# Performance work log

Measured on AMD Instinct MI355X. Metric: run time of the kernel, lower is better.

## Reference

```python
import jax, jax.numpy as jnp
import numpy as np

B, S, D = 4, 4096, 1024

def setup_inputs() -> dict:
    key = jax.random.key(0)
    ks = jax.random.split(key, 7)
    s = 1.0 / np.sqrt(D)
    return {
        "x":   jax.random.normal(ks[0], (B, S, D), dtype=jnp.float32),
        "Wq":  jax.random.uniform(ks[1], (D, D), jnp.float32, -s, s),
        "bq":  jax.random.uniform(ks[2], (D,),   jnp.float32, -s, s),
        "Wk":  jax.random.uniform(ks[3], (D, D), jnp.float32, -s, s),
        "bk":  jax.random.uniform(ks[4], (D,),   jnp.float32, -s, s),
        "Wv":  jax.random.uniform(ks[5], (D, D), jnp.float32, -s, s),
        "bv":  jax.random.uniform(ks[6], (D,),   jnp.float32, -s, s),
    }

def reference(x, Wq, bq, Wk, bk, Wv, bv):
    # Linear projections (torch Linear: x @ W.T + b; here W stored as [in, out])
    Q = jnp.einsum('bsd,df->bsf', x, Wq) + bq
    K = jnp.einsum('bsd,df->bsf', x, Wk) + bk
    V = jnp.einsum('bsd,df->bsf', x, Wv) + bv
    scale = 1.0 / jnp.sqrt(jnp.asarray(D, dtype=jnp.float32))
    scores = jnp.einsum('bqd,bkd->bqk', Q, K) * scale  # [B, S, S]
    attn = jax.nn.softmax(scores, axis=-1)
    return jnp.einsum('bqk,bkd->bqd', attn, V)
```

## Files before the change

### kernel.cpp

```cpp
#include <hip/hip_runtime.h>
#include <hip/hip_bf16.h>
#include <stdint.h>


typedef __attribute__((ext_vector_type(8))) short bf16x8;
typedef __attribute__((ext_vector_type(4))) float f32x4;

static __device__ __forceinline__ unsigned short f2b(float f) {
  union { float f; unsigned u; } x; x.f = f;
  unsigned u = x.u;
  u += 0x7fffu + ((u >> 16) & 1u);
  return (unsigned short)(u >> 16);
}
static __device__ __forceinline__ float b2f(unsigned short s) {
  union { unsigned u; float f; } x; x.u = ((unsigned)s) << 16;
  return x.f;
}

static __device__ __forceinline__ void gl_lds16(const void* g, void* l) {
  __builtin_amdgcn_global_load_lds(
      (const __attribute__((address_space(1))) void*)(uintptr_t)(g),
      (__attribute__((address_space(3))) void*)(uint32_t)(uintptr_t)(l),
      16, 0, 0);
}

__global__ void convert_x(const float* __restrict__ in,
                          unsigned short* __restrict__ out, int n8) {
  int i = blockIdx.x * blockDim.x + threadIdx.x;
  if (i >= n8) return;
  const float4* p = (const float4*)in + (size_t)i * 2;
  float4 a = p[0], b = p[1];
  bf16x8 o;
  o[0] = (short)f2b(a.x); o[1] = (short)f2b(a.y);
  o[2] = (short)f2b(a.z); o[3] = (short)f2b(a.w);
  o[4] = (short)f2b(b.x); o[5] = (short)f2b(b.y);
  o[6] = (short)f2b(b.z); o[7] = (short)f2b(b.w);
  ((bf16x8*)out)[i] = o;
}

__global__ void transpose_w(const float* __restrict__ in,
                            unsigned short* __restrict__ out) {
  __shared__ float tile[32][33];
  const int tx = threadIdx.x;
  const int x = blockIdx.x * 32 + tx;
  const int y0 = blockIdx.y * 32;
  for (int j = threadIdx.y; j < 32; j += 8)
    tile[j][tx] = in[(size_t)(y0 + j) * 1024 + x];
  __syncthreads();
  const int ox = blockIdx.y * 32 + tx;
  const int oy0 = blockIdx.x * 32;
  for (int j = threadIdx.y; j < 32; j += 8)
    out[(size_t)(oy0 + j) * 1024 + ox] = f2b(tile[tx][j]);
}

template <int OUTF>
__global__ __launch_bounds__(512, 2)
void gemm256(const unsigned short* __restrict__ A, long lda, long sAz,
             const unsigned short* __restrict__ B, long ldb, long sBz,
             void* __restrict__ Cv, long ldc, long sCz,
             const float* __restrict__ bias, int bias_mode,
             int K, float alpha) {
  __shared__ __align__(16) unsigned short As[2][2][8192];
  __shared__ __align__(16) unsigned short Bs[2][2][8192];

  const unsigned gx = gridDim.x, gy = gridDim.y;
  const unsigned nwg = gx * gy * gridDim.z;
  const unsigned hwid = (blockIdx.z * gy + blockIdx.y) * gx + blockIdx.x;
  unsigned tile = hwid;
  if ((nwg & 7u) == 0u) tile = (hwid & 7u) * (nwg >> 3) + (hwid >> 3);
  const unsigned bxi = tile % gx;
  const unsigned byi = (tile / gx) % gy;
  const unsigned bzi = tile / (gx * gy);

  const int t = threadIdx.x;
  const int wid = t >> 6, lane = t & 63;
  const int wm = wid >> 2, wn = wid & 3;
  const int fr = lane & 15, fq = lane >> 4;
  const long bm = (long)byi * 256;
  const long bn = (long)bxi * 256;
  const unsigned short* Ab = A + (size_t)bzi * sAz;
  const unsigned short* Bb = B + (size_t)bzi * sBz;

  const int srow = t >> 2;
  const int soct8 = (((t & 3) ^ ((t >> 3) & 3))) * 8;
  const unsigned short* AgS = Ab + (bm + srow) * lda + soct8;
  const unsigned short* BgS = Bb + (bn + srow) * ldb + soct8;
  const int dstw = wid * 512;
  const int rs16 = (fq ^ ((fr >> 1) & 3)) << 4;

  const int NT = K >> 6;
  f32x4 acc[8][4] = {};

  auto stg = [&](const unsigned short* GS, long ld, unsigned short* region,
                 int kt, int kh) {
    const unsigned short* s0 = GS + (size_t)kt * 64 + kh * 32;
    gl_lds16(s0, region + dstw);
    gl_lds16(s0 + (size_t)128 * ld, region + 4096 + dstw);
  };
  auto rdA = [&](int buf, int kh, int i) {
    return *(const bf16x8*)((const char*)&As[buf][kh][0] +
                            (wm * 128 + i * 16 + fr) * 64 + rs16);
  };
  auto rdB = [&](int buf, int kh, int j) {
    return *(const bf16x8*)((const char*)&Bs[buf][kh][0] +
                            (wn * 64 + j * 16 + fr) * 64 + rs16);
  };

  stg(AgS, lda, &As[0][0][0], 0, 0); stg(BgS, ldb, &Bs[0][0][0], 0, 0);
  stg(AgS, lda, &As[0][1][0], 0, 1); stg(BgS, ldb, &Bs[0][1][0], 0, 1);
  asm volatile("s_waitcnt vmcnt(4)" ::: "memory");
  asm volatile("s_barrier" ::: "memory");

#define PHASE(kh)                                                             \
  do {                                                                        \
    if (tt + 1 < NT) {                                                        \
      stg(AgS, lda, &As[nb][kh][0], tt + 1, kh);                              \
      stg(BgS, ldb, &Bs[nb][kh][0], tt + 1, kh);                              \
    }                                                                         \
    bf16x8 bfr[4], ar[2], arn[2];                                             \
    _Pragma("unroll")                                                         \
    for (int j = 0; j < 4; ++j) bfr[j] = rdB(cb, kh, j);                      \
    ar[0] = rdA(cb, kh, 0); ar[1] = rdA(cb, kh, 1);                           \
    __builtin_amdgcn_s_setprio(1);                                            \
    _Pragma("unroll")                                                         \
    for (int p = 0; p < 4; ++p) {                                             \
      if (p < 3) {                                                            \
        arn[0] = rdA(cb, kh, p * 2 + 2);                                      \
        arn[1] = rdA(cb, kh, p * 2 + 3);                                      \
      }                                                                       \
      _Pragma("unroll")                                                       \
      for (int ii = 0; ii < 2; ++ii)                                          \
        _Pragma("unroll")                                                     \
        for (int j = 0; j < 4; ++j)                                           \
          acc[p * 2 + ii][j] = __builtin_amdgcn_mfma_f32_16x16x32_bf16(       \
              ar[ii], bfr[j], acc[p * 2 + ii][j], 0, 0, 0);                   \
      if (p < 3) { ar[0] = arn[0]; ar[1] = arn[1]; }                          \
    }                                                                         \
    __builtin_amdgcn_s_setprio(0);                                            \
  } while (0)

  for (int tt = 0; tt < NT; ++tt) {
    const int cb = tt & 1, nb = (tt + 1) & 1;
    if (tt > 0) {
      asm volatile("s_waitcnt vmcnt(4)" ::: "memory");
      asm volatile("s_barrier" ::: "memory");
    }
    PHASE(0);
    if (tt + 1 < NT) {
      asm volatile("s_waitcnt vmcnt(4)" ::: "memory");
    } else {
      asm volatile("s_waitcnt vmcnt(0)" ::: "memory");
    }
    asm volatile("s_barrier" ::: "memory");
    PHASE(1);
  }
#undef PHASE

  char* Cb = (char*)Cv + (size_t)bzi * sCz * (OUTF ? 4 : 2);
  const long crow0 = bm + wm * 128 + fq * 4;
  const long ccol0 = bn + wn * 64 + fr;
#pragma unroll
  for (int i = 0; i < 8; ++i) {
#pragma unroll
    for (int j = 0; j < 4; ++j) {
      const long col = ccol0 + j * 16;
      float badd_c = (bias_mode == 1) ? bias[col] : 0.0f;
#pragma unroll
      for (int r = 0; r < 4; ++r) {
        const long row = crow0 + i * 16 + r;
        float v = acc[i][j][r] * alpha + badd_c;
        if (bias_mode == 2) v += bias[row];
        if (OUTF)
          ((float*)Cb)[row * ldc + col] = v;
        else
          ((unsigned short*)Cb)[row * ldc + col] = f2b(v);
      }
    }
  }
}

__global__ __launch_bounds__(256)
void softmax_rows(unsigned short* __restrict__ S) {
  const int t = threadIdx.x;
  unsigned short* row = S + (size_t)blockIdx.x * 4096;
  const bf16x8* p = (const bf16x8*)row;
  bf16x8 u0 = p[t * 2], u1 = p[t * 2 + 1];

  float v[16];
  float m = -1e30f;
#pragma unroll
  for (int j = 0; j < 8; j++) { v[j] = b2f((unsigned short)u0[j]); }
#pragma unroll
  for (int j = 0; j < 8; j++) { v[8 + j] = b2f((unsigned short)u1[j]); }
#pragma unroll
  for (int j = 0; j < 16; j++) m = fmaxf(m, v[j]);

#pragma unroll
  for (int off = 32; off > 0; off >>= 1) m = fmaxf(m, __shfl_xor(m, off));
  __shared__ float redm[4];
  if ((t & 63) == 0) redm[t >> 6] = m;
  __syncthreads();
  m = fmaxf(fmaxf(redm[0], redm[1]), fmaxf(redm[2], redm[3]));

  float s = 0.0f;
#pragma unroll
  for (int j = 0; j < 16; j++) { v[j] = __expf(v[j] - m); s += v[j]; }
#pragma unroll
  for (int off = 32; off > 0; off >>= 1) s += __shfl_xor(s, off);
  __shared__ float reds[4];
  if ((t & 63) == 0) reds[t >> 6] = s;
  __syncthreads();
  s = reds[0] + reds[1] + reds[2] + reds[3];
  const float inv = 1.0f / s;

  bf16x8 o0, o1;
#pragma unroll
  for (int j = 0; j < 8; j++) o0[j] = (short)f2b(v[j] * inv);
#pragma unroll
  for (int j = 0; j < 8; j++) o1[j] = (short)f2b(v[8 + j] * inv);
  bf16x8* q = (bf16x8*)row;
  q[t * 2] = o0;
  q[t * 2 + 1] = o1;
}

extern "C" void kernel_launch(void* const* d_in, const int* in_sizes, int n_in,
                              void* d_out, int out_size, void* d_ws,
                              size_t ws_size, hipStream_t stream) {
  const float* x  = (const float*)d_in[0];
  const float* Wq = (const float*)d_in[1];
  const float* bq = (const float*)d_in[2];
  const float* Wk = (const float*)d_in[3];
  const float* bk = (const float*)d_in[4];
  const float* Wv = (const float*)d_in[5];
  const float* bv = (const float*)d_in[6];
  float* out = (float*)d_out;

  const int Bb = 4, S = 4096, D = 1024;
  const long BS = (long)Bb * S;
  const size_t MiB = 1u << 20;

  char* base = (char*)d_ws;
  unsigned short* Wqt = (unsigned short*)(base);
  unsigned short* Wkt = (unsigned short*)(base + 2 * MiB);
  unsigned short* Wvt = (unsigned short*)(base + 4 * MiB);
  unsigned short* Qb  = (unsigned short*)(base + 6 * MiB);
  unsigned short* Kb  = (unsigned short*)(base + 38 * MiB);
  unsigned short* Vt  = (unsigned short*)(base + 70 * MiB);
  unsigned short* xb  = (unsigned short*)(base + 102 * MiB);
  unsigned short* Sb  = xb;
  const bool batched = ws_size >= (size_t)(102 + 128) * MiB;

  const int n8 = (int)(BS * D / 8);
  convert_x<<<n8 / 256, 256, 0, stream>>>(x, xb, n8);

  dim3 tb(32, 8), tg(32, 32);
  transpose_w<<<tg, tb, 0, stream>>>(Wq, Wqt);
  transpose_w<<<tg, tb, 0, stream>>>(Wk, Wkt);
  transpose_w<<<tg, tb, 0, stream>>>(Wv, Wvt);

  gemm256<0><<<dim3(D / 256, BS / 256, 1), 512, 0, stream>>>(
      xb, D, 0, Wqt, D, 0, Qb, D, 0, bq, 1, D, 1.0f);
  gemm256<0><<<dim3(D / 256, BS / 256, 1), 512, 0, stream>>>(
      xb, D, 0, Wkt, D, 0, Kb, D, 0, bk, 1, D, 1.0f);
  gemm256<0><<<dim3(BS / 256, D / 256, 1), 512, 0, stream>>>(
      Wvt, D, 0, xb, D, 0, Vt, BS, 0, bv, 2, D, 1.0f);

  const float scale = 0.03125f;
  if (batched) {
    gemm256<0><<<dim3(S / 256, S / 256, Bb), 512, 0, stream>>>(
        Qb, D, (long)S * D, Kb, D, (long)S * D, Sb, S, (long)S * S,
        nullptr, 0, D, scale);
    softmax_rows<<<Bb * S, 256, 0, stream>>>(Sb);
    gemm256<1><<<dim3(D / 256, S / 256, Bb), 512, 0, stream>>>(
        Sb, S, (long)S * S, Vt, BS, (long)S, out, D, (long)S * D,
        nullptr, 0, S, 1.0f);
  } else {
    for (int b = 0; b < Bb; b++) {
      const unsigned short* Qp = Qb + (long)b * S * D;
      const unsigned short* Kp = Kb + (long)b * S * D;
      gemm256<0><<<dim3(S / 256, S / 256, 1), 512, 0, stream>>>(
          Qp, D, 0, Kp, D, 0, Sb, S, 0, nullptr, 0, D, scale);
      softmax_rows<<<S, 256, 0, stream>>>(Sb);
      gemm256<1><<<dim3(D / 256, S / 256, 1), 512, 0, stream>>>(
          Sb, S, 0, Vt + (long)b * S, BS, 0, out + (long)b * S * D, D, 0,
          nullptr, 0, S, 1.0f);
    }
  }
}
```

Measured before the change: 483.5 us.

## Restructure GEMM main loop into 8-phase ping-pong schedule with staggered A/B loads

Replaces the two-half-K double-buffered loop with a schedule that processes two K-tiles per iteration in four sub-phases each. Each sub-phase issues a slice of the next global-to-LDS copies, then hits a barrier, then runs its MFMAs. The LDS layout changes from split 32-wide K halves to full 64-wide rows with an XOR swizzle on 16-byte chunks. The goal is to interleave the memory traffic more finely with the MFMA work and keep B prefetched further ahead. In exchange there are more barriers per tile, and the hand-written vmcnt accounting is fragile. The loop also assumes NT is even.

Measured after the change: 460.4 us. 4.8% less time.

```diff
diff --git a/kernel.cpp b/kernel.cpp
--- a/kernel.cpp
+++ b/kernel.cpp
@@ -53,6 +53,8 @@
     out[(size_t)(oy0 + j) * 1024 + ox] = f2b(tile[tx][j]);
 }
 
+#define MFMA16(a, b, c) __builtin_amdgcn_mfma_f32_16x16x32_bf16(a, b, c, 0, 0, 0)
+
 template <int OUTF>
 __global__ __launch_bounds__(512, 2)
 void gemm256(const unsigned short* __restrict__ A, long lda, long sAz,
@@ -60,17 +62,17 @@
              void* __restrict__ Cv, long ldc, long sCz,
              const float* __restrict__ bias, int bias_mode,
              int K, float alpha) {
-  __shared__ __align__(16) unsigned short As[2][2][8192];
-  __shared__ __align__(16) unsigned short Bs[2][2][8192];
+  __shared__ __align__(16) unsigned short As[2][256 * 64];
+  __shared__ __align__(16) unsigned short Bs[2][256 * 64];
 
   const unsigned gx = gridDim.x, gy = gridDim.y;
   const unsigned nwg = gx * gy * gridDim.z;
   const unsigned hwid = (blockIdx.z * gy + blockIdx.y) * gx + blockIdx.x;
-  unsigned tile = hwid;
-  if ((nwg & 7u) == 0u) tile = (hwid & 7u) * (nwg >> 3) + (hwid >> 3);
-  const unsigned bxi = tile % gx;
-  const unsigned byi = (tile / gx) % gy;
-  const unsigned bzi = tile / (gx * gy);
+  unsigned tileid = hwid;
+  if ((nwg & 7u) == 0u) tileid = (hwid & 7u) * (nwg >> 3) + (hwid >> 3);
+  const unsigned bxi = tileid % gx;
+  const unsigned byi = (tileid / gx) % gy;
+  const unsigned bzi = tileid / (gx * gy);
 
   const int t = threadIdx.x;
   const int wid = t >> 6, lane = t & 63;
@@ -81,78 +83,96 @@
   const unsigned short* Ab = A + (size_t)bzi * sAz;
   const unsigned short* Bb = B + (size_t)bzi * sBz;
 
-  const int srow = t >> 2;
-  const int soct8 = (((t & 3) ^ ((t >> 3) & 3))) * 8;
-  const unsigned short* AgS = Ab + (bm + srow) * lda + soct8;
-  const unsigned short* BgS = Bb + (bn + srow) * ldb + soct8;
-  const int dstw = wid * 512;
-  const int rs16 = (fq ^ ((fr >> 1) & 3)) << 4;
+  const int sr = t >> 3;
+  const int scol = 8 * ((t & 7) ^ (sr & 7));
+  const unsigned short* AgS = Ab + (bm + sr) * lda + scol;
+  const unsigned short* BgS = Bb + (bn + sr) * ldb + scol;
+  const int ldsw = wid * 512;
 
   const int NT = K >> 6;
   f32x4 acc[8][4] = {};
 
-  auto stg = [&](const unsigned short* GS, long ld, unsigned short* region,
-                 int kt, int kh) {
-    const unsigned short* s0 = GS + (size_t)kt * 64 + kh * 32;
-    gl_lds16(s0, region + dstw);
-    gl_lds16(s0 + (size_t)128 * ld, region + 4096 + dstw);
+  auto SH = [&](const unsigned short* GS, long ld, int kt, int h,
+                unsigned short* dstbuf) {
+    const unsigned short* s = GS + (size_t)(h * 128) * ld + (size_t)kt * 64;
+    gl_lds16(s, dstbuf + h * 128 * 64 + ldsw);
+    gl_lds16(s + (size_t)64 * ld, dstbuf + (h * 128 + 64) * 64 + ldsw);
   };
-  auto rdA = [&](int buf, int kh, int i) {
-    return *(const bf16x8*)((const char*)&As[buf][kh][0] +
-                            (wm * 128 + i * 16 + fr) * 64 + rs16);
+
+  auto rdA = [&](int buf, int m, int kh) {
+    const int row = wm * 128 + m * 16 + fr;
+    const int inb = (kh * 64 + fq * 16) ^ ((fr & 7) << 4);
+    return *(const bf16x8*)((const char*)&As[buf][0] + row * 128 + inb);
   };
-  auto rdB = [&](int buf, int kh, int j) {
-    return *(const bf16x8*)((const char*)&Bs[buf][kh][0] +
-                            (wn * 64 + j * 16 + fr) * 64 + rs16);
+  auto rdB = [&](int buf, int j, int kh) {
+    const int row = wn * 64 + j * 16 + fr;
+    const int inb = (kh * 64 + fq * 16) ^ ((fr & 7) << 4);
+    return *(const bf16x8*)((const char*)&Bs[buf][0] + row * 128 + inb);
   };
 
-  stg(AgS, lda, &As[0][0][0], 0, 0); stg(BgS, ldb, &Bs[0][0][0], 0, 0);
-  stg(AgS, lda, &As[0][1][0], 0, 1); stg(BgS, ldb, &Bs[0][1][0], 0, 1);
-  asm volatile("s_waitcnt vmcnt(4)" ::: "memory");
-  asm volatile("s_barrier" ::: "memory");
-
-#define PHASE(kh)                                                             \
-  do {                                                                        \
-    if (tt + 1 < NT) {                                                        \
-      stg(AgS, lda, &As[nb][kh][0], tt + 1, kh);                              \
-      stg(BgS, ldb, &Bs[nb][kh][0], tt + 1, kh);                              \
+#define PHASE(CB, P, STAGES, WAITS)                                           \
+  {                                                                           \
+    if ((P) == 0) {                                                           \
+      _Pragma("unroll") for (int j = 0; j < 4; ++j) {                         \
+        bfr[j][0] = rdB(CB, j, 0);                                            \
+        bfr[j][1] = rdB(CB, j, 1);                                            \
+      }                                                                       \
     }                                                                         \
-    bf16x8 bfr[4], ar[2], arn[2];                                             \
-    _Pragma("unroll")                                                         \
-    for (int j = 0; j < 4; ++j) bfr[j] = rdB(cb, kh, j);                      \
-    ar[0] = rdA(cb, kh, 0); ar[1] = rdA(cb, kh, 1);                           \
+    bf16x8 a00 = rdA(CB, 2 * (P), 0), a01 = rdA(CB, 2 * (P), 1);              \
+    bf16x8 a10 = rdA(CB, 2 * (P) + 1, 0), a11 = rdA(CB, 2 * (P) + 1, 1);      \
+    STAGES;                                                                   \
+    if ((P) == 0) asm volatile("s_waitcnt lgkmcnt(8)" ::: "memory");          \
+    __builtin_amdgcn_s_barrier();                                             \
+    asm volatile("s_waitcnt lgkmcnt(0)" ::: "memory");                        \
+    __builtin_amdgcn_sched_barrier(0);                                        \
     __builtin_amdgcn_s_setprio(1);                                            \
-    _Pragma("unroll")                                                         \
-    for (int p = 0; p < 4; ++p) {                                             \
-      if (p < 3) {                                                            \
-        arn[0] = rdA(cb, kh, p * 2 + 2);                                      \
-        arn[1] = rdA(cb, kh, p * 2 + 3);                                      \
-      }                                                                       \
-      _Pragma("unroll")                                                       \
-      for (int ii = 0; ii < 2; ++ii)                                          \
-        _Pragma("unroll")                                                     \
-        for (int j = 0; j < 4; ++j)                                           \
-          acc[p * 2 + ii][j] = __builtin_amdgcn_mfma_f32_16x16x32_bf16(       \
-              ar[ii], bfr[j], acc[p * 2 + ii][j], 0, 0, 0);                   \
-      if (p < 3) { ar[0] = arn[0]; ar[1] = arn[1]; }                          \
+    _Pragma("unroll") for (int j = 0; j < 4; ++j) {                           \
+      acc[2 * (P)][j] = MFMA16(a00, bfr[j][0], acc[2 * (P)][j]);              \
+      acc[2 * (P)][j] = MFMA16(a01, bfr[j][1], acc[2 * (P)][j]);              \
+      acc[2 * (P) + 1][j] = MFMA16(a10, bfr[j][0], acc[2 * (P) + 1][j]);      \
+      acc[2 * (P) + 1][j] = MFMA16(a11, bfr[j][1], acc[2 * (P) + 1][j]);      \
     }                                                                         \
     __builtin_amdgcn_s_setprio(0);                                            \
-  } while (0)
-
-  for (int tt = 0; tt < NT; ++tt) {
-    const int cb = tt & 1, nb = (tt + 1) & 1;
-    if (tt > 0) {
-      asm volatile("s_waitcnt vmcnt(4)" ::: "memory");
-      asm volatile("s_barrier" ::: "memory");
+    WAITS;                                                                    \
+    __builtin_amdgcn_s_barrier();                                             \
+  }
+
+  SH(AgS, lda, 0, 0, &As[0][0]);
+  SH(AgS, lda, 0, 1, &As[0][0]);
+  SH(BgS, ldb, 0, 0, &Bs[0][0]);
+  SH(BgS, ldb, 0, 1, &Bs[0][0]);
+  if (1 < NT) {
+    SH(BgS, ldb, 1, 0, &Bs[1][0]);
+    SH(BgS, ldb, 1, 1, &Bs[1][0]);
+  }
+  asm volatile("s_waitcnt vmcnt(0)" ::: "memory");
+  __builtin_amdgcn_s_barrier();
+
+  for (int it = 0; it < (NT >> 1); ++it) {
+    const int T = 2 * it;
+    {
+      bf16x8 bfr[4][2];
+      PHASE(0, 0, { if (T + 1 < NT) SH(AgS, lda, T + 1, 0, &As[1][0]); }, {});
+      PHASE(0, 1, {
+        if (T + 1 < NT) SH(AgS, lda, T + 1, 1, &As[1][0]);
+        if (T + 2 < NT) SH(BgS, ldb, T + 2, 0, &Bs[0][0]);
+      }, {});
+      PHASE(0, 2, { if (T + 2 < NT) SH(BgS, ldb, T + 2, 1, &Bs[0][0]); }, {});
+      PHASE(0, 3, {}, {
+        if (T + 2 < NT)
+          asm volatile("s_waitcnt vmcnt(4)" ::: "memory");
+        else
+          asm volatile("s_waitcnt vmcnt(0)" ::: "memory");
+      });
     }
-    PHASE(0);
-    if (tt + 1 < NT) {
-      asm volatile("s_waitcnt vmcnt(4)" ::: "memory");
-    } else {
-      asm volatile("s_waitcnt vmcnt(0)" ::: "memory");
+    {
+      bf16x8 bfr[4][2];
+      PHASE(1, 0, { if (T + 2 < NT) SH(AgS, lda, T + 2, 0, &As[0][0]); }, {});
+      PHASE(1, 1, { if (T + 2 < NT) SH(AgS, lda, T + 2, 1, &As[0][0]); }, {});
+      PHASE(1, 2, { if (T + 3 < NT) SH(BgS, ldb, T + 3, 0, &Bs[1][0]); }, {});
+      PHASE(1, 3, { if (T + 3 < NT) SH(BgS, ldb, T + 3, 1, &Bs[1][0]); },
+            { asm volatile("s_waitcnt vmcnt(4)" ::: "memory"); });
     }
-    asm volatile("s_barrier" ::: "memory");
-    PHASE(1);
   }
 #undef PHASE
 
```
